# Optimization experiments

Measured on AMD Instinct MI355X. Metric: run time of the kernel, lower is better.

The kernel has to match this reference:

```python
import jax, jax.numpy as jnp
import numpy as np

B, T_SEQ, STATE, DIM_IN, DIM_K, DIM_V, LAYER = 8, 2048, 128, 1024, 64, 64, 4
T = T_SEQ + 2 * STATE  # 2304
LAMBDA_INIT = 0.8 - 0.6 * float(np.exp(-0.3 * LAYER))
NEG = -1e30


def setup_inputs() -> dict:
    key = jax.random.key(0)
    ks = jax.random.split(key, 20)
    def w(k, shape):
        return jax.random.normal(k, shape, dtype=jnp.float32) * 0.02
    inp = {"x": jax.random.normal(ks[0], (B, T, DIM_IN), dtype=jnp.float32)}
    # projection weights stored as (in, out) so y = x @ W
    inp["Wq"] = w(ks[1], (DIM_IN, 2 * DIM_K)); inp["Wk"] = w(ks[2], (DIM_IN, 2 * DIM_K)); inp["Wv"] = w(ks[3], (DIM_IN, 2 * DIM_V))
    inp["Wq_ss"] = w(ks[4], (DIM_IN, 2 * DIM_K)); inp["Wk_ss"] = w(ks[5], (DIM_IN, 2 * DIM_K)); inp["Wv_ss"] = w(ks[6], (DIM_IN, 2 * DIM_V))
    inp["Wq_se"] = w(ks[7], (DIM_IN, 2 * DIM_K)); inp["Wk_se"] = w(ks[8], (DIM_IN, 2 * DIM_K)); inp["Wv_se"] = w(ks[9], (DIM_IN, 2 * DIM_V))
    # layernorm params (torch defaults: ones/zeros)
    inp["g_in"] = jnp.ones((DIM_IN,), jnp.float32); inp["b_in"] = jnp.zeros((DIM_IN,), jnp.float32)
    inp["g_ss"] = jnp.ones((DIM_IN,), jnp.float32); inp["b_ss"] = jnp.zeros((DIM_IN,), jnp.float32)
    inp["g_se"] = jnp.ones((DIM_IN,), jnp.float32); inp["b_se"] = jnp.zeros((DIM_IN,), jnp.float32)
    inp["g_out"] = jnp.ones((2 * DIM_V,), jnp.float32); inp["b_out"] = jnp.zeros((2 * DIM_V,), jnp.float32)
    # lambda gate params
    inp["lq1"] = jax.random.normal(ks[10], (1, DIM_K), jnp.float32)
    inp["lq2"] = jax.random.normal(ks[11], (1, DIM_K), jnp.float32)
    inp["lk1"] = jax.random.normal(ks[12], (DIM_K, 1), jnp.float32)
    inp["lk2"] = jax.random.normal(ks[13], (DIM_K, 1), jnp.float32)
    return inp


def _ln(z, g, b, eps=1e-5):
    m = jnp.mean(z, axis=-1, keepdims=True)
    v = jnp.mean((z - m) ** 2, axis=-1, keepdims=True)
    return (z - m) * jax.lax.rsqrt(v + eps) * g + b


def reference(x, Wq, Wk, Wv, Wq_ss, Wk_ss, Wv_ss, Wq_se, Wk_se, Wv_se,
              g_in, b_in, g_ss, b_ss, g_se, b_se, g_out, b_out,
              lq1, lq2, lk1, lk2):
    # extract_state: split off state tokens at both ends
    xs, xm, xe = x[:, :STATE], x[:, STATE:-STATE], x[:, -STATE:]
    xm = _ln(xm, g_in, b_in)
    xs = _ln(xs, g_ss, b_ss)
    xe = _ln(xe, g_se, b_se)
    q = jnp.concatenate([xs @ Wq_ss, xm @ Wq, xe @ Wq_se], axis=1)  # (B,T,2K)
    k = jnp.concatenate([xs @ Wk_ss, xm @ Wk, xe @ Wk_se], axis=1)
    v = jnp.concatenate([xs @ Wv_ss, xm @ Wv, xe @ Wv_se], axis=1)  # (B,T,2V)
    q1, q2 = q[..., :DIM_K], q[..., DIM_K:]
    k1, k2 = k[..., :DIM_K], k[..., DIM_K:]
    scale = 1.0 / np.sqrt(DIM_K)
    t = q.shape[1]
    causal = jnp.triu(jnp.full((t, t), NEG, dtype=q.dtype), k=1)  # (T,T)
    s1 = jnp.einsum('btd,bsd->bts', q1, k1) * scale + causal
    s2 = jnp.einsum('btd,bsd->bts', q2, k2) * scale + causal
    a1 = jax.nn.softmax(s1, axis=-1)
    a2 = jax.nn.softmax(s2, axis=-1)
    o1 = jnp.einsum('bts,bsd->btd', a1, v)
    o2 = jnp.einsum('bts,bsd->btd', a2, v)
    lam = (jnp.exp(lq1 @ lk1) - jnp.exp(lq2 @ lk2))[0, 0] + LAMBDA_INIT
    att = o1 - lam * o2
    return _ln(att, g_out, b_out)
```

## Files before the change

### kernel.cpp

```cpp
#include <hip/hip_runtime.h>
#include <hip/hip_bf16.h>
#include <stdint.h>

#define B_ 8
#define T_ 2304
#define DIN 1024
#define LAMBDA_INIT_F 0.6192834728526788f

typedef __bf16 bf16x8 __attribute__((ext_vector_type(8)));
typedef float f32x4 __attribute__((ext_vector_type(4)));

__device__ __forceinline__ unsigned short f2bf(float f) {
    union { float f; unsigned int u; } v; v.f = f;
    unsigned int u = v.u;
    unsigned int r = (u + 0x7FFFu + ((u >> 16) & 1u)) >> 16;
    return (unsigned short)r;
}

__device__ __forceinline__ unsigned int pack2bf(float lo, float hi) {
    return ((unsigned int)f2bf(hi) << 16) | (unsigned int)f2bf(lo);
}

__device__ __forceinline__ float bf2f(unsigned short u) {
    union { unsigned int u; float f; } v; v.u = ((unsigned int)u) << 16;
    return v.f;
}

__device__ __forceinline__ void gload16(const void* g, void* l) {
    __builtin_amdgcn_global_load_lds(
        (const __attribute__((address_space(1))) unsigned int*)g,
        (__attribute__((address_space(3))) unsigned int*)l,
        16, 0, 0);
}

__global__ __launch_bounds__(256) void k_wtrans(
    const float* w0, const float* w1, const float* w2,
    const float* w3, const float* w4, const float* w5,
    const float* w6, const float* w7, const float* w8,
    unsigned short* __restrict__ wt)
{
    __shared__ float tile[64][65];
    int bx = blockIdx.x;
    int mat = bx >> 5;
    int tl = bx & 31;
    int tx = tl & 15;
    int ty = tl >> 4;
    const float* srcs[9] = {w0, w1, w2, w3, w4, w5, w6, w7, w8};
    const float* src = srcs[mat];
    int k0 = tx * 64, c0 = ty * 64;
    int t = threadIdx.x;
    int r = t >> 2, cg = (t & 3) << 4;
    const float* p = src + (size_t)(k0 + r) * 128 + c0 + cg;
#pragma unroll
    for (int i = 0; i < 4; ++i) {
        float4 v = *(const float4*)(p + i * 4);
        tile[r][cg + i * 4 + 0] = v.x;
        tile[r][cg + i * 4 + 1] = v.y;
        tile[r][cg + i * 4 + 2] = v.z;
        tile[r][cg + i * 4 + 3] = v.w;
    }
    __syncthreads();
    int seg = mat / 3, m = mat % 3;
    int crow = seg * 384 + m * 128 + c0 + r;
    unsigned short* dst = wt + (size_t)crow * 1024 + k0 + cg;
    __align__(16) unsigned short ob[16];
#pragma unroll
    for (int i = 0; i < 16; ++i) ob[i] = f2bf(tile[cg + i][r]);
    *(uint4*)(dst) = *(const uint4*)(ob);
    *(uint4*)(dst + 8) = *(const uint4*)(ob + 8);
}

__global__ __launch_bounds__(256) void k_ln(
    const float* __restrict__ x,
    const float* __restrict__ g_in, const float* __restrict__ b_in,
    const float* __restrict__ g_ss, const float* __restrict__ b_ss,
    const float* __restrict__ g_se, const float* __restrict__ b_se,
    unsigned short* __restrict__ xbf)
{
    int row = (blockIdx.x << 2) + (threadIdx.x >> 6);
    int l = threadIdx.x & 63;
    int t = row % T_;
    const float* gv; const float* bv;
    if (t < 128)       { gv = g_ss; bv = b_ss; }
    else if (t < 2176) { gv = g_in; bv = b_in; }
    else               { gv = g_se; bv = b_se; }
    const float* xp = x + (size_t)row * DIN + l * 4;
    float4 v0 = *(const float4*)(xp);
    float4 v1 = *(const float4*)(xp + 256);
    float4 v2 = *(const float4*)(xp + 512);
    float4 v3 = *(const float4*)(xp + 768);
    float s  = v0.x + v0.y + v0.z + v0.w + v1.x + v1.y + v1.z + v1.w
             + v2.x + v2.y + v2.z + v2.w + v3.x + v3.y + v3.z + v3.w;
    float s2 = v0.x*v0.x + v0.y*v0.y + v0.z*v0.z + v0.w*v0.w
             + v1.x*v1.x + v1.y*v1.y + v1.z*v1.z + v1.w*v1.w
             + v2.x*v2.x + v2.y*v2.y + v2.z*v2.z + v2.w*v2.w
             + v3.x*v3.x + v3.y*v3.y + v3.z*v3.z + v3.w*v3.w;
#pragma unroll
    for (int off = 1; off <= 32; off <<= 1) {
        s  += __shfl_xor(s,  off);
        s2 += __shfl_xor(s2, off);
    }
    float mean = s * (1.f / 1024.f);
    float rstd = rsqrtf(s2 * (1.f / 1024.f) - mean * mean + 1e-5f);
    unsigned short* op = xbf + (size_t)row * DIN + l * 4;
    const float* gp = gv + l * 4;
    const float* bp = bv + l * 4;
#pragma unroll
    for (int k = 0; k < 4; ++k) {
        float4 vv = (k == 0) ? v0 : (k == 1) ? v1 : (k == 2) ? v2 : v3;
        float4 gk = *(const float4*)(gp + k * 256);
        float4 bk = *(const float4*)(bp + k * 256);
        uint2 o;
        o.x = pack2bf((vv.x - mean) * rstd * gk.x + bk.x,
                      (vv.y - mean) * rstd * gk.y + bk.y);
        o.y = pack2bf((vv.z - mean) * rstd * gk.z + bk.z,
                      (vv.w - mean) * rstd * gk.w + bk.w);
        *(uint2*)(op + k * 256) = o;
    }
}

__global__ __launch_bounds__(512, 4) void k_proj2(
    const unsigned short* __restrict__ xbf,
    const unsigned short* __restrict__ wt,
    unsigned short* __restrict__ qo,
    unsigned short* __restrict__ ko,
    unsigned short* __restrict__ vto)
{
    __shared__ __align__(16) char smem[81920];

    int bid = blockIdx.x;
    int mt = bid >> 1, ch = bid & 1;
    int bb = mt / 18, tt = mt % 18;
    int seg = (tt == 0) ? 0 : ((tt < 17) ? 1 : 2);
    size_t arow0 = (size_t)mt * 128;
    int ncol0 = ch * 192;
    int wrow0 = seg * 384 + ncol0;

    int tid = threadIdx.x;
    int w = tid >> 6, l = tid & 63;
    int wr = w >> 2, wc = w & 3;
    int g4 = l >> 4, cr = l & 15;

    int rA0 = tid >> 3, cS = (tid & 7) << 4;
    const char* srcA0 = (const char*)xbf + (arow0 + rA0) * 2048 + cS;
    const char* srcA1 = srcA0 + (size_t)64 * 2048;
    int dA0 = rA0 * 128 + (cS ^ ((rA0 & 7) << 4));
    int dA1 = dA0 + 64 * 128;
    const char* srcW0 = (const char*)wt + (size_t)(wrow0 + rA0) * 2048 + cS;
    const char* srcW1 = srcW0 + (size_t)64 * 2048;
    const char* srcW2 = srcW0 + (size_t)128 * 2048;
    int dW0 = dA0, dW1 = dA0 + 64 * 128, dW2 = dA0 + 128 * 128;

    {
        uint4 a0 = *(const uint4*)srcA0;
        uint4 a1 = *(const uint4*)srcA1;
        uint4 w0 = *(const uint4*)srcW0;
        uint4 w1 = *(const uint4*)srcW1;
        uint4 w2 = *(const uint4*)srcW2;
        *(uint4*)(smem + dA0) = a0;
        *(uint4*)(smem + dA1) = a1;
        *(uint4*)(smem + 32768 + dW0) = w0;
        *(uint4*)(smem + 32768 + dW1) = w1;
        *(uint4*)(smem + 32768 + dW2) = w2;
    }
    __syncthreads();

    f32x4 acc[4][3] = {};
    for (int ks = 0; ks < 16; ++ks) {
        bool pf = (ks < 15);
        uint4 pa0, pa1, pw0, pw1, pw2;
        if (pf) {
            size_t o = (size_t)(ks + 1) * 128;
            pa0 = *(const uint4*)(srcA0 + o);
            pa1 = *(const uint4*)(srcA1 + o);
            pw0 = *(const uint4*)(srcW0 + o);
            pw1 = *(const uint4*)(srcW1 + o);
            pw2 = *(const uint4*)(srcW2 + o);
        }
        const char* Ab = smem + (ks & 1) * 16384;
        const char* Wb = smem + 32768 + (ks & 1) * 24576;
        __builtin_amdgcn_s_setprio(1);
#pragma unroll
        for (int kk = 0; kk < 2; ++kk) {
            int kb = kk * 64 + g4 * 16;
            bf16x8 af[4];
#pragma unroll
            for (int r4 = 0; r4 < 4; ++r4) {
                int rr = wr * 64 + r4 * 16 + cr;
                af[r4] = *(const bf16x8*)(Ab + rr * 128 + (kb ^ ((rr & 7) << 4)));
            }
            bf16x8 bfr[3];
#pragma unroll
            for (int nt = 0; nt < 3; ++nt) {
                int c = wc * 48 + nt * 16 + cr;
                bfr[nt] = *(const bf16x8*)(Wb + c * 128 + (kb ^ ((c & 7) << 4)));
            }
#pragma unroll
            for (int r4 = 0; r4 < 4; ++r4)
#pragma unroll
                for (int nt = 0; nt < 3; ++nt)
                    acc[r4][nt] = __builtin_amdgcn_mfma_f32_16x16x32_bf16(af[r4], bfr[nt], acc[r4][nt], 0, 0, 0);
        }
        __builtin_amdgcn_s_setprio(0);
        __syncthreads();
        if (pf) {
            char* An = smem + ((ks + 1) & 1) * 16384;
            char* Wn = smem + 32768 + ((ks + 1) & 1) * 24576;
            *(uint4*)(An + dA0) = pa0;
            *(uint4*)(An + dA1) = pa1;
            *(uint4*)(Wn + dW0) = pw0;
            *(uint4*)(Wn + dW1) = pw1;
            *(uint4*)(Wn + dW2) = pw2;
        }
        __syncthreads();
    }

#pragma unroll
    for (int r4 = 0; r4 < 4; ++r4) {
        size_t grow = arow0 + wr * 64 + r4 * 16 + g4 * 4;
#pragma unroll
        for (int nt = 0; nt < 3; ++nt) {
            int c = ncol0 + wc * 48 + nt * 16 + cr;
            f32x4 a = acc[r4][nt];
            if (c < 128) {
#pragma unroll
                for (int g = 0; g < 4; ++g)
                    qo[(grow + g) * 128 + c] = f2bf(a[g]);
            } else if (c < 256) {
#pragma unroll
                for (int g = 0; g < 4; ++g)
                    ko[(grow + g) * 128 + (c - 128)] = f2bf(a[g]);
            } else {
                int cv = c - 256;
                int trow = tt * 128 + wr * 64 + r4 * 16 + g4 * 4;
                uint2 o;
                o.x = pack2bf(a[0], a[1]);
                o.y = pack2bf(a[2], a[3]);
                *(uint2*)(vto + ((size_t)bb * 128 + cv) * T_ + trow) = o;
            }
        }
    }
}

__global__ __launch_bounds__(256, 3) void k_attn(
    const unsigned short* __restrict__ qp_,
    const unsigned short* __restrict__ kp_,
    const unsigned short* __restrict__ vp_,
    const float* __restrict__ lq1, const float* __restrict__ lq2,
    const float* __restrict__ lk1, const float* __restrict__ lk2,
    const float* __restrict__ g_out, const float* __restrict__ b_out,
    unsigned short* __restrict__ opart,
    float* __restrict__ mlpart,
    float* __restrict__ out)
{
    __shared__ __align__(16) char smem[32768];

    int bid = blockIdx.x;
    int b = bid & 7;
    int u = 125 - (bid >> 3);
    int j, ci;
    if (u < 6) { j = u; ci = 0; }
    else {
        int v = u - 6;
        int g, base;
        if (v < 12)      { g = 0; base = 0;  }
        else if (v < 30) { g = 1; base = 12; }
        else if (v < 54) { g = 2; base = 30; }
        else if (v < 84) { g = 3; base = 54; }
        else             { g = 4; base = 84; }
        int w2 = v - base;
        int per = g + 2;
        int qd = w2 / per;
        j = 6 * (g + 1) + qd;
        ci = w2 - qd * per;
    }
    int nch = (j + 6) / 6;
    int c0 = ci * 6;
    int ntile = min(6, j + 1 - c0);
    int t0 = j * 64;

    int tid = threadIdx.x;
    int qg = tid >> 6;
    int l = tid & 63;
    int g4 = l >> 4, q = l & 15;
    int q_g = t0 + qg * 16 + q;

    int rbK = qg * 4 + (l >> 4);
    const char* kSrc0 = (const char*)kp_ + ((size_t)b * T_ + rbK) * 256
                      + (((l & 15) << 4) ^ ((rbK & 7) << 4));
    int rbV = qg * 8 + (l >> 3);
    const char* vSrc0 = (const char*)vp_ + ((size_t)b * 128 + rbV) * (T_ * 2)
                      + (((l & 7) << 4) ^ ((rbV & 7) << 4));
    char* ldsK = smem + qg * 1024;
    char* ldsV = smem + 16384 + qg * 1024;

    bf16x8 qf[2][2];
#pragma unroll
    for (int br = 0; br < 2; ++br)
#pragma unroll
        for (int h = 0; h < 2; ++h)
            qf[br][h] = *(const bf16x8*)(qp_ + ((size_t)b * T_ + q_g) * 128 + br * 64 + h * 32 + g4 * 8);

    {
        const char* kS = kSrc0 + (size_t)c0 * 16384;
        const char* vS = vSrc0 + (size_t)c0 * 128;
#pragma unroll
        for (int c = 0; c < 4; ++c) {
            gload16(kS + c * 4096, ldsK + c * 4096);
            gload16(vS + (size_t)c * 147456, ldsV + c * 4096);
        }
    }
    __syncthreads();

    float mrun[2] = {-1e30f, -1e30f};
    float lrun[2] = {0.f, 0.f};
    f32x4 oacc[2][8] = {};
    const char* Kb = smem;
    const char* Vb = smem + 16384;

    for (int t = 0; t < ntile; ++t) {
        int kt = c0 + t;
        bool diag = (kt == j);
        bool pfv = (t + 1 < ntile);
        unsigned int pk[2][4][2];
#pragma unroll
        for (int br = 0; br < 2; ++br) {
            f32x4 s[4] = {};
            __builtin_amdgcn_s_setprio(1);
#pragma unroll
            for (int h = 0; h < 2; ++h) {
#pragma unroll
                for (int t4 = 0; t4 < 4; ++t4) {
                    int rk = t4 * 16 + q;
                    bf16x8 kf = *(const bf16x8*)(Kb + rk * 256 + ((br * 128 + h * 64 + g4 * 16) ^ ((rk & 7) << 4)));
                    s[t4] = __builtin_amdgcn_mfma_f32_16x16x32_bf16(kf, qf[br][h], s[t4], 0, 0, 0);
                }
            }
            __builtin_amdgcn_s_setprio(0);
            float sv[16];
            float mx = -1e30f;
#pragma unroll
            for (int t4 = 0; t4 < 4; ++t4)
#pragma unroll
                for (int r = 0; r < 4; ++r) {
                    float v = s[t4][r] * 0.125f;
                    if (diag) {
                        int kv_g = kt * 64 + t4 * 16 + g4 * 4 + r;
                        if (kv_g > q_g) v = -1e30f;
                    }
                    sv[t4 * 4 + r] = v;
                    mx = fmaxf(mx, v);
                }
            mx = fmaxf(mx, __shfl_xor(mx, 16));
            mx = fmaxf(mx, __shfl_xor(mx, 32));
            float mn;
            if (__all(mx <= mrun[br] + 8.f)) {
                mn = mrun[br];
            } else {
                mn = fmaxf(mrun[br], mx);
                float sf = __expf(mrun[br] - mn);
                mrun[br] = mn;
                lrun[br] *= sf;
#pragma unroll
                for (int dblk = 0; dblk < 8; ++dblk)
#pragma unroll
                    for (int r = 0; r < 4; ++r)
                        oacc[br][dblk][r] *= sf;
            }
            float pr[16];
            float rs = 0.f;
#pragma unroll
            for (int i = 0; i < 16; ++i) {
                pr[i] = __expf(sv[i] - mn);
                rs += pr[i];
            }
            rs += __shfl_xor(rs, 16);
            rs += __shfl_xor(rs, 32);
            lrun[br] += rs;
#pragma unroll
            for (int t4 = 0; t4 < 4; ++t4) {
                pk[br][t4][0] = pack2bf(pr[t4 * 4 + 0], pr[t4 * 4 + 1]);
                pk[br][t4][1] = pack2bf(pr[t4 * 4 + 2], pr[t4 * 4 + 3]);
            }
        }
        __syncthreads();
        if (pfv) {
            const char* kS = kSrc0 + (size_t)(kt + 1) * 16384;
#pragma unroll
            for (int c = 0; c < 4; ++c)
                gload16(kS + c * 4096, ldsK + c * 4096);
        }
#pragma unroll
        for (int h = 0; h < 2; ++h) {
            bf16x8 pb[2];
            int s0 = q + (((g4 * 2) & 3) << 4);
            int s1 = q + (((g4 * 2 + 1) & 3) << 4);
            int sel = g4 >> 1;
#pragma unroll
            for (int br = 0; br < 2; ++br) {
                unsigned int m0a = (unsigned int)__shfl((int)pk[br][0 + 2 * h][0], s0);
                unsigned int m0b = (unsigned int)__shfl((int)pk[br][1 + 2 * h][0], s0);
                unsigned int m1a = (unsigned int)__shfl((int)pk[br][0 + 2 * h][1], s0);
                unsigned int m1b = (unsigned int)__shfl((int)pk[br][1 + 2 * h][1], s0);
                unsigned int m2a = (unsigned int)__shfl((int)pk[br][0 + 2 * h][0], s1);
                unsigned int m2b = (unsigned int)__shfl((int)pk[br][1 + 2 * h][0], s1);
                unsigned int m3a = (unsigned int)__shfl((int)pk[br][0 + 2 * h][1], s1);
                unsigned int m3b = (unsigned int)__shfl((int)pk[br][1 + 2 * h][1], s1);
                union { unsigned int uv[4]; bf16x8 v; } pu;
                pu.uv[0] = sel ? m0b : m0a;
                pu.uv[1] = sel ? m1b : m1a;
                pu.uv[2] = sel ? m2b : m2a;
                pu.uv[3] = sel ? m3b : m3a;
                pb[br] = pu.v;
            }
            __builtin_amdgcn_s_setprio(1);
#pragma unroll
            for (int dblk = 0; dblk < 8; ++dblk) {
                int rv = dblk * 16 + q;
                bf16x8 vf = *(const bf16x8*)(Vb + rv * 128 + ((h * 64 + g4 * 16) ^ ((rv & 7) << 4)));
                oacc[0][dblk] = __builtin_amdgcn_mfma_f32_16x16x32_bf16(vf, pb[0], oacc[0][dblk], 0, 0, 0);
                oacc[1][dblk] = __builtin_amdgcn_mfma_f32_16x16x32_bf16(vf, pb[1], oacc[1][dblk], 0, 0, 0);
            }
            __builtin_amdgcn_s_setprio(0);
        }
        __syncthreads();
        if (pfv) {
            const char* vS = vSrc0 + (size_t)(kt + 1) * 128;
#pragma unroll
            for (int c = 0; c < 4; ++c)
                gload16(vS + (size_t)c * 147456, ldsV + c * 4096);
        }
    }

    int row = qg * 16 + q;
    if (nch == 1) {
        float pa = lq1[l] * lk1[l];
        float pb2 = lq2[l] * lk2[l];
#pragma unroll
        for (int off = 32; off >= 1; off >>= 1) {
            pa += __shfl_xor(pa, off);
            pb2 += __shfl_xor(pb2, off);
        }
        float lam = __expf(pa) - __expf(pb2) + LAMBDA_INIT_F;

        float att[8][4];
        float sm = 0.f;
        float inv1 = 1.f / lrun[0], inv2 = 1.f / lrun[1];
#pragma unroll
        for (int dblk = 0; dblk < 8; ++dblk)
#pragma unroll
            for (int r = 0; r < 4; ++r) {
                float a = oacc[0][dblk][r] * inv1 - lam * (oacc[1][dblk][r] * inv2);
                att[dblk][r] = a;
                sm += a;
            }
        sm += __shfl_xor(sm, 16);
        sm += __shfl_xor(sm, 32);
        float mean = sm * (1.f / 128.f);
        float sv2 = 0.f;
#pragma unroll
        for (int dblk = 0; dblk < 8; ++dblk)
#pragma unroll
            for (int r = 0; r < 4; ++r) {
                float d = att[dblk][r] - mean;
                sv2 += d * d;
            }
        sv2 += __shfl_xor(sv2, 16);
        sv2 += __shfl_xor(sv2, 32);
        float rstd = rsqrtf(sv2 * (1.f / 128.f) + 1e-5f);

        float* orow = out + ((size_t)b * T_ + q_g) * 128;
#pragma unroll
        for (int dblk = 0; dblk < 8; ++dblk) {
            int d0 = dblk * 16 + g4 * 4;
            float4 o;
            o.x = (att[dblk][0] - mean) * rstd * g_out[d0 + 0] + b_out[d0 + 0];
            o.y = (att[dblk][1] - mean) * rstd * g_out[d0 + 1] + b_out[d0 + 1];
            o.z = (att[dblk][2] - mean) * rstd * g_out[d0 + 2] + b_out[d0 + 2];
            o.w = (att[dblk][3] - mean) * rstd * g_out[d0 + 3] + b_out[d0 + 3];
            *(float4*)(orow + d0) = o;
        }
    } else {
        int g2 = (j - 6) / 6;
        int off = 6 * g2 * (g2 + 3) / 2 + (j - 6 - 6 * g2) * (g2 + 2);
        int slot = b * 120 + off + ci;
        char* ob = (char*)opart + (size_t)slot * 32768;
#pragma unroll
        for (int br = 0; br < 2; ++br) {
#pragma unroll
            for (int dblk = 0; dblk < 8; ++dblk) {
                uint2 o;
                o.x = pack2bf(oacc[br][dblk][0], oacc[br][dblk][1]);
                o.y = pack2bf(oacc[br][dblk][2], oacc[br][dblk][3]);
                *(uint2*)(ob + br * 16384 + row * 256 + (dblk * 16 + g4 * 4) * 2) = o;
            }
            if (g4 == 0) {
                float2 mlv;
                mlv.x = mrun[br];
                mlv.y = lrun[br];
                *(float2*)(mlpart + ((size_t)slot * 128 + br * 64 + row) * 2) = mlv;
            }
        }
    }
}

__global__ __launch_bounds__(512) void k_merge(
    const unsigned short* __restrict__ opart,
    const float* __restrict__ mlpart,
    const float* __restrict__ lq1, const float* __restrict__ lq2,
    const float* __restrict__ lk1, const float* __restrict__ lk2,
    const float* __restrict__ g_out, const float* __restrict__ b_out,
    float* __restrict__ out)
{
    int bid = blockIdx.x;
    int b = bid & 7;
    int j = 6 + (bid >> 3);
    int nch = (j + 6) / 6;
    int g2 = (j - 6) / 6;
    int slotb = b * 120 + 6 * g2 * (g2 + 3) / 2 + (j - 6 - 6 * g2) * (g2 + 2);
    int tid = threadIdx.x;
    int row = tid >> 3;
    int d0 = (tid & 7) * 16;
    int l = tid & 63;

    float pa = lq1[l] * lk1[l];
    float pb = lq2[l] * lk2[l];
#pragma unroll
    for (int off = 32; off >= 1; off >>= 1) {
        pa += __shfl_xor(pa, off);
        pb += __shfl_xor(pb, off);
    }
    float lam = __expf(pa) - __expf(pb) + LAMBDA_INIT_F;

    float res[2][16];
#pragma unroll
    for (int br = 0; br < 2; ++br) {
        float mv0 = -1e30f, mv1 = -1e30f, mv2 = -1e30f,
              mv3 = -1e30f, mv4 = -1e30f, mv5 = -1e30f;
        float lv0 = 0.f, lv1 = 0.f, lv2 = 0.f, lv3 = 0.f, lv4 = 0.f, lv5 = 0.f;
        {
            const float* p0 = mlpart + ((size_t)slotb * 128 + br * 64 + row) * 2;
            mv0 = p0[0]; lv0 = p0[1];
            const float* p1 = mlpart + ((size_t)(slotb + 1) * 128 + br * 64 + row) * 2;
            mv1 = p1[0]; lv1 = p1[1];
            if (nch > 2) { const float* p = mlpart + ((size_t)(slotb + 2) * 128 + br * 64 + row) * 2; mv2 = p[0]; lv2 = p[1]; }
            if (nch > 3) { const float* p = mlpart + ((size_t)(slotb + 3) * 128 + br * 64 + row) * 2; mv3 = p[0]; lv3 = p[1]; }
            if (nch > 4) { const float* p = mlpart + ((size_t)(slotb + 4) * 128 + br * 64 + row) * 2; mv4 = p[0]; lv4 = p[1]; }
            if (nch > 5) { const float* p = mlpart + ((size_t)(slotb + 5) * 128 + br * 64 + row) * 2; mv5 = p[0]; lv5 = p[1]; }
        }
        float mstar = fmaxf(fmaxf(fmaxf(mv0, mv1), fmaxf(mv2, mv3)), fmaxf(mv4, mv5));
        float w0 = __expf(mv0 - mstar);
        float w1 = __expf(mv1 - mstar);
        float w2 = (nch > 2) ? __expf(mv2 - mstar) : 0.f;
        float w3 = (nch > 3) ? __expf(mv3 - mstar) : 0.f;
        float w4 = (nch > 4) ? __expf(mv4 - mstar) : 0.f;
        float w5 = (nch > 5) ? __expf(mv5 - mstar) : 0.f;
        float lsum = w0 * lv0 + w1 * lv1 + w2 * lv2 + w3 * lv3 + w4 * lv4 + w5 * lv5;

        float acc[16] = {};
#pragma unroll
        for (int c = 0; c < 6; ++c) {
            if (c >= nch) break;
            float wc = (c == 0) ? w0 : (c == 1) ? w1 : (c == 2) ? w2
                     : (c == 3) ? w3 : (c == 4) ? w4 : w5;
            const char* ob = (const char*)opart + (size_t)(slotb + c) * 32768
                           + br * 16384 + row * 256 + d0 * 2;
            uint4 v0 = *(const uint4*)(ob);
            uint4 v1 = *(const uint4*)(ob + 16);
            const unsigned int vv[8] = {v0.x, v0.y, v0.z, v0.w, v1.x, v1.y, v1.z, v1.w};
#pragma unroll
            for (int i = 0; i < 8; ++i) {
                acc[i * 2]     += wc * bf2f((unsigned short)(vv[i] & 0xFFFF));
                acc[i * 2 + 1] += wc * bf2f((unsigned short)(vv[i] >> 16));
            }
        }
        float inv = 1.f / lsum;
#pragma unroll
        for (int i = 0; i < 16; ++i) res[br][i] = acc[i] * inv;
    }

    float att[16];
    float sm = 0.f;
#pragma unroll
    for (int i = 0; i < 16; ++i) {
        att[i] = res[0][i] - lam * res[1][i];
        sm += att[i];
    }
    sm += __shfl_xor(sm, 1);
    sm += __shfl_xor(sm, 2);
    sm += __shfl_xor(sm, 4);
    float mean = sm * (1.f / 128.f);
    float sv2 = 0.f;
#pragma unroll
    for (int i = 0; i < 16; ++i) {
        float d = att[i] - mean;
        sv2 += d * d;
    }
    sv2 += __shfl_xor(sv2, 1);
    sv2 += __shfl_xor(sv2, 2);
    sv2 += __shfl_xor(sv2, 4);
    float rstd = rsqrtf(sv2 * (1.f / 128.f) + 1e-5f);

    float* orow = out + ((size_t)b * T_ + j * 64 + row) * 128 + d0;
#pragma unroll
    for (int k = 0; k < 4; ++k) {
        float4 o;
        o.x = (att[k * 4 + 0] - mean) * rstd * g_out[d0 + k * 4 + 0] + b_out[d0 + k * 4 + 0];
        o.y = (att[k * 4 + 1] - mean) * rstd * g_out[d0 + k * 4 + 1] + b_out[d0 + k * 4 + 1];
        o.z = (att[k * 4 + 2] - mean) * rstd * g_out[d0 + k * 4 + 2] + b_out[d0 + k * 4 + 2];
        o.w = (att[k * 4 + 3] - mean) * rstd * g_out[d0 + k * 4 + 3] + b_out[d0 + k * 4 + 3];
        *(float4*)(orow + k * 4) = o;
    }
}

extern "C" void kernel_launch(void* const* d_in, const int* in_sizes, int n_in,
                              void* d_out, int out_size, void* d_ws, size_t ws_size,
                              hipStream_t stream) {
    (void)in_sizes; (void)n_in; (void)out_size; (void)ws_size;
    const float* x = (const float*)d_in[0];
    char* ws = (char*)d_ws;
    unsigned short* wt  = (unsigned short*)ws;
    unsigned short* xbf = (unsigned short*)(ws + 2359296);
    unsigned short* qo  = (unsigned short*)(ws + 40108032);
    unsigned short* ko  = (unsigned short*)(ws + 44826624);
    unsigned short* vto = (unsigned short*)(ws + 49545216);
    unsigned short* opart = (unsigned short*)(ws + 2359296);
    float*          mlpart = (float*)(ws + 2359296 + 31457280);

    hipLaunchKernelGGL(k_wtrans, dim3(288), dim3(256), 0, stream,
        (const float*)d_in[4], (const float*)d_in[5], (const float*)d_in[6],
        (const float*)d_in[1], (const float*)d_in[2], (const float*)d_in[3],
        (const float*)d_in[7], (const float*)d_in[8], (const float*)d_in[9], wt);

    hipLaunchKernelGGL(k_ln, dim3(4608), dim3(256), 0, stream,
        x,
        (const float*)d_in[10], (const float*)d_in[11],
        (const float*)d_in[12], (const float*)d_in[13],
        (const float*)d_in[14], (const float*)d_in[15],
        xbf);

    hipLaunchKernelGGL(k_proj2, dim3(288), dim3(512), 0, stream,
        xbf, wt, qo, ko, vto);

    hipLaunchKernelGGL(k_attn, dim3(1008), dim3(256), 0, stream,
        qo, ko, vto,
        (const float*)d_in[18], (const float*)d_in[19],
        (const float*)d_in[20], (const float*)d_in[21],
        (const float*)d_in[16], (const float*)d_in[17],
        opart, mlpart,
        (float*)d_out);

    hipLaunchKernelGGL(k_merge, dim3(240), dim3(512), 0, stream,
        opart, mlpart,
        (const float*)d_in[18], (const float*)d_in[19],
        (const float*)d_in[20], (const float*)d_in[21],
        (const float*)d_in[16], (const float*)d_in[17],
        (float*)d_out);
}
```

Baseline: 117.8 us.

## Fold softmax scale and log2e into Q, permute K rows to drop P shuffles

Pre-multiplies Q by scale*log2(e) in the projection epilogue so the attention kernel can use exp2 directly and skip the per-score multiply. It reorders how K rows are loaded into LDS so the score MFMA output layout already matches the PV operand layout, which removes the eight cross-lane shuffles and selects per P fragment. It also switches packing to the hardware bf16 conversion and widens the lazy-rescale threshold to match the base-2 domain. The risks are a subtle mismatch between the causal mask index remap and the new K row order, and a change in rounding behaviour.

```diff
diff --git a/kernel.cpp b/kernel.cpp
--- a/kernel.cpp
+++ b/kernel.cpp
@@ -6,6 +6,7 @@
 #define T_ 2304
 #define DIN 1024
 #define LAMBDA_INIT_F 0.6192834728526788f
+#define QSCALE 0.1803368801111137f
 
 typedef __bf16 bf16x8 __attribute__((ext_vector_type(8)));
 typedef float f32x4 __attribute__((ext_vector_type(4)));
@@ -19,6 +20,12 @@
 
 __device__ __forceinline__ unsigned int pack2bf(float lo, float hi) {
     return ((unsigned int)f2bf(hi) << 16) | (unsigned int)f2bf(lo);
+}
+
+__device__ __forceinline__ unsigned int cvt2bf(float lo, float hi) {
+    union { __bf16 h[2]; unsigned int u; } v;
+    v.h[0] = (__bf16)lo; v.h[1] = (__bf16)hi;
+    return v.u;
 }
 
 __device__ __forceinline__ float bf2f(unsigned short u) {
@@ -225,7 +232,7 @@
             if (c < 128) {
 #pragma unroll
                 for (int g = 0; g < 4; ++g)
-                    qo[(grow + g) * 128 + c] = f2bf(a[g]);
+                    qo[(grow + g) * 128 + c] = f2bf(a[g] * QSCALE);
             } else if (c < 256) {
 #pragma unroll
                 for (int g = 0; g < 4; ++g)
@@ -285,9 +292,10 @@
     int g4 = l >> 4, q = l & 15;
     int q_g = t0 + qg * 16 + q;
 
-    int rbK = qg * 4 + (l >> 4);
-    const char* kSrc0 = (const char*)kp_ + ((size_t)b * T_ + rbK) * 256
-                      + (((l & 15) << 4) ^ ((rbK & 7) << 4));
+    int ldsRowK = qg * 4 + (l >> 4);
+    const char* kSrc0 = (const char*)kp_
+                      + ((size_t)b * T_ + qg * 8 + (l >> 4)) * 256
+                      + (((l & 15) << 4) ^ ((ldsRowK & 7) << 4));
     int rbV = qg * 8 + (l >> 3);
     const char* vSrc0 = (const char*)vp_ + ((size_t)b * 128 + rbV) * (T_ * 2)
                       + (((l & 7) << 4) ^ ((rbV & 7) << 4));
@@ -304,11 +312,13 @@
     {
         const char* kS = kSrc0 + (size_t)c0 * 16384;
         const char* vS = vSrc0 + (size_t)c0 * 128;
-#pragma unroll
-        for (int c = 0; c < 4; ++c) {
-            gload16(kS + c * 4096, ldsK + c * 4096);
+        gload16(kS,        ldsK);
+        gload16(kS + 8192, ldsK + 4096);
+        gload16(kS + 1024, ldsK + 8192);
+        gload16(kS + 9216, ldsK + 12288);
+#pragma unroll
+        for (int c = 0; c < 4; ++c)
             gload16(vS + (size_t)c * 147456, ldsV + c * 4096);
-        }
     }
     __syncthreads();
 
@@ -343,9 +353,9 @@
             for (int t4 = 0; t4 < 4; ++t4)
 #pragma unroll
                 for (int r = 0; r < 4; ++r) {
-                    float v = s[t4][r] * 0.125f;
+                    float v = s[t4][r];
                     if (diag) {
-                        int kv_g = kt * 64 + t4 * 16 + g4 * 4 + r;
+                        int kv_g = kt * 64 + (t4 & 1) * 32 + g4 * 8 + (t4 >> 1) * 4 + r;
                         if (kv_g > q_g) v = -1e30f;
                     }
                     sv[t4 * 4 + r] = v;
@@ -354,11 +364,11 @@
             mx = fmaxf(mx, __shfl_xor(mx, 16));
             mx = fmaxf(mx, __shfl_xor(mx, 32));
             float mn;
-            if (__all(mx <= mrun[br] + 8.f)) {
+            if (__all(mx <= mrun[br] + 11.5f)) {
                 mn = mrun[br];
             } else {
                 mn = fmaxf(mrun[br], mx);
-                float sf = __expf(mrun[br] - mn);
+                float sf = exp2f(mrun[br] - mn);
                 mrun[br] = mn;
                 lrun[br] *= sf;
 #pragma unroll
@@ -371,7 +381,7 @@
             float rs = 0.f;
 #pragma unroll
             for (int i = 0; i < 16; ++i) {
-                pr[i] = __expf(sv[i] - mn);
+                pr[i] = exp2f(sv[i] - mn);
                 rs += pr[i];
             }
             rs += __shfl_xor(rs, 16);
@@ -379,38 +389,28 @@
             lrun[br] += rs;
 #pragma unroll
             for (int t4 = 0; t4 < 4; ++t4) {
-                pk[br][t4][0] = pack2bf(pr[t4 * 4 + 0], pr[t4 * 4 + 1]);
-                pk[br][t4][1] = pack2bf(pr[t4 * 4 + 2], pr[t4 * 4 + 3]);
+                pk[br][t4][0] = cvt2bf(pr[t4 * 4 + 0], pr[t4 * 4 + 1]);
+                pk[br][t4][1] = cvt2bf(pr[t4 * 4 + 2], pr[t4 * 4 + 3]);
             }
         }
         __syncthreads();
         if (pfv) {
             const char* kS = kSrc0 + (size_t)(kt + 1) * 16384;
-#pragma unroll
-            for (int c = 0; c < 4; ++c)
-                gload16(kS + c * 4096, ldsK + c * 4096);
+            gload16(kS,        ldsK);
+            gload16(kS + 8192, ldsK + 4096);
+            gload16(kS + 1024, ldsK + 8192);
+            gload16(kS + 9216, ldsK + 12288);
         }
 #pragma unroll
         for (int h = 0; h < 2; ++h) {
             bf16x8 pb[2];
-            int s0 = q + (((g4 * 2) & 3) << 4);
-            int s1 = q + (((g4 * 2 + 1) & 3) << 4);
-            int sel = g4 >> 1;
 #pragma unroll
             for (int br = 0; br < 2; ++br) {
-                unsigned int m0a = (unsigned int)__shfl((int)pk[br][0 + 2 * h][0], s0);
-                unsigned int m0b = (unsigned int)__shfl((int)pk[br][1 + 2 * h][0], s0);
-                unsigned int m1a = (unsigned int)__shfl((int)pk[br][0 + 2 * h][1], s0);
-                unsigned int m1b = (unsigned int)__shfl((int)pk[br][1 + 2 * h][1], s0);
-                unsigned int m2a = (unsigned int)__shfl((int)pk[br][0 + 2 * h][0], s1);
-                unsigned int m2b = (unsigned int)__shfl((int)pk[br][1 + 2 * h][0], s1);
-                unsigned int m3a = (unsigned int)__shfl((int)pk[br][0 + 2 * h][1], s1);
-                unsigned int m3b = (unsigned int)__shfl((int)pk[br][1 + 2 * h][1], s1);
                 union { unsigned int uv[4]; bf16x8 v; } pu;
-                pu.uv[0] = sel ? m0b : m0a;
-                pu.uv[1] = sel ? m1b : m1a;
-                pu.uv[2] = sel ? m2b : m2a;
-                pu.uv[3] = sel ? m3b : m3a;
+                pu.uv[0] = pk[br][h][0];
+                pu.uv[1] = pk[br][h][1];
+                pu.uv[2] = pk[br][2 + h][0];
+                pu.uv[3] = pk[br][2 + h][1];
                 pb[br] = pu.v;
             }
             __builtin_amdgcn_s_setprio(1);
@@ -549,12 +549,12 @@
             if (nch > 5) { const float* p = mlpart + ((size_t)(slotb + 5) * 128 + br * 64 + row) * 2; mv5 = p[0]; lv5 = p[1]; }
         }
         float mstar = fmaxf(fmaxf(fmaxf(mv0, mv1), fmaxf(mv2, mv3)), fmaxf(mv4, mv5));
-        float w0 = __expf(mv0 - mstar);
-        float w1 = __expf(mv1 - mstar);
-        float w2 = (nch > 2) ? __expf(mv2 - mstar) : 0.f;
-        float w3 = (nch > 3) ? __expf(mv3 - mstar) : 0.f;
-        float w4 = (nch > 4) ? __expf(mv4 - mstar) : 0.f;
-        float w5 = (nch > 5) ? __expf(mv5 - mstar) : 0.f;
+        float w0 = exp2f(mv0 - mstar);
+        float w1 = exp2f(mv1 - mstar);
+        float w2 = (nch > 2) ? exp2f(mv2 - mstar) : 0.f;
+        float w3 = (nch > 3) ? exp2f(mv3 - mstar) : 0.f;
+        float w4 = (nch > 4) ? exp2f(mv4 - mstar) : 0.f;
+        float w5 = (nch > 5) ? exp2f(mv5 - mstar) : 0.f;
         float lsum = w0 * lv0 + w1 * lv1 + w2 * lv2 + w3 * lv3 + w4 * lv4 + w5 * lv5;
 
         float acc[16] = {};
```

New measurement: 113.3 us. -3.8%, faster.
